# Optimization experiments

Hardware: AMD Instinct MI355X
Metric: run time of the kernel (lower is better)

The kernel has to match this reference:

```python
import jax, jax.numpy as jnp
import numpy as np

K_EXPERTS = 2  # init kwarg k_experts

def _glu_mlp(x, up_w, gate_w, down_w):
    # gated MLP: down( up(x) * GELU(gate(x)) ), exact-erf GELU matching torch nn.GELU()
    h = (x @ up_w) * jax.nn.gelu(x @ gate_w, approximate=False)
    return h @ down_w

def setup_inputs() -> dict:
    key = jax.random.key(0)
    ks = jax.random.split(key, 8)
    B, S, D, I, E = 2, 2048, 1024, 512, 8
    sc = 0.02
    return {
        "x": jax.random.normal(ks[0], (B, S, D), jnp.float32),
        "gate_w": jax.random.normal(ks[1], (E, D), jnp.float32) * sc,
        "up_w": jax.random.normal(ks[2], (E, D, I), jnp.float32) * sc,
        "gproj_w": jax.random.normal(ks[3], (E, D, I), jnp.float32) * sc,
        "down_w": jax.random.normal(ks[4], (E, I, D), jnp.float32) * sc,
        "shared_up_w": jax.random.normal(ks[5], (D, I), jnp.float32) * sc,
        "shared_gate_w": jax.random.normal(ks[6], (D, I), jnp.float32) * sc,
        "shared_down_w": jax.random.normal(ks[7], (I, D), jnp.float32) * sc,
    }

def reference(x, gate_w, up_w, gproj_w, down_w, shared_up_w, shared_gate_w, shared_down_w):
    B, S, D = x.shape
    E = gate_w.shape[0]
    xf = x.reshape(-1, D)                      # [T, D]
    T = xf.shape[0]

    # --- SigmaGate: softmax over expert logits, top-k, renormalize ---
    logits = xf @ gate_w.T                     # [T, E]
    scores = jax.nn.softmax(logits, axis=-1)
    topk_w, topk_idx = jax.lax.top_k(scores, K_EXPERTS)   # [T, k]
    topk_w = topk_w / (topk_w.sum(axis=-1, keepdims=True) + 1e-20)

    # combine weights as dense [T, E] (topk indices are distinct per token)
    combine = jnp.zeros((T, E), xf.dtype).at[jnp.arange(T)[:, None], topk_idx].add(topk_w)

    # --- experts: scan over E, accumulate weighted expert outputs ---
    def step(acc, ws):
        uw, gw, dw, ce = ws                    # ce: [T] combine weight for this expert
        y_e = _glu_mlp(xf, uw, gw, dw)         # [T, D]
        return acc + ce[:, None] * y_e, None

    y, _ = jax.lax.scan(step, jnp.zeros_like(xf), (up_w, gproj_w, down_w, combine.T))

    # --- shared expert on identity ---
    y = y + _glu_mlp(xf, shared_up_w, shared_gate_w, shared_down_w)
    return y.reshape(B, S, D)
```

## Files before the change

kernel.cpp:

```cpp
#include <hip/hip_runtime.h>
#include <hip/hip_bf16.h>
#include <math.h>

#define T_TOK 4096
#define D_DIM 1024
#define I_DIM 512
#define E_EXP 8
#define KSEL 2
#define NPAIR (T_TOK * KSEL)
#define ROUTED_CAP 9216
#define SHARED_BASE ROUTED_CAP
#define RTOT (ROUTED_CAP + T_TOK)
#define MAXTILES 104
#define GRID_G (MAXTILES * 8)

typedef __bf16 bf16x8 __attribute__((ext_vector_type(8)));
typedef float f32x4 __attribute__((ext_vector_type(4)));
typedef unsigned short ushort8 __attribute__((ext_vector_type(8)));

constexpr size_t SZ_XB  = (size_t)T_TOK * D_DIM * 2;
constexpr size_t SZ_UG  = (size_t)E_EXP * 2 * I_DIM * D_DIM * 2;
constexpr size_t SZ_DT  = (size_t)E_EXP * I_DIM * D_DIM * 2;
constexpr size_t SZ_SUG = (size_t)2 * I_DIM * D_DIM * 2;
constexpr size_t SZ_SDT = (size_t)I_DIM * D_DIM * 2;
constexpr size_t SZ_H   = (size_t)RTOT * I_DIM * 2;
constexpr size_t SZ_Y   = (size_t)RTOT * D_DIM * 2;

constexpr size_t OFF_XB   = 0;
constexpr size_t OFF_UG   = OFF_XB  + SZ_XB;
constexpr size_t OFF_DT   = OFF_UG  + SZ_UG;
constexpr size_t OFF_SUG  = OFF_DT  + SZ_DT;
constexpr size_t OFF_SDT  = OFF_SUG + SZ_SUG;
constexpr size_t OFF_H    = OFF_SDT + SZ_SDT;
constexpr size_t OFF_Y    = OFF_H   + SZ_H;
constexpr size_t OFF_TOPKI= OFF_Y   + SZ_Y;
constexpr size_t OFF_TOPKW= OFF_TOPKI + (size_t)NPAIR * 4;
constexpr size_t OFF_INV  = OFF_TOPKW + (size_t)NPAIR * 4;
constexpr size_t OFF_PERM = OFF_INV   + (size_t)NPAIR * 4;
constexpr size_t OFF_META = OFF_PERM  + (size_t)RTOT * 4;

__device__ __forceinline__ unsigned short f2bf(float f) {
  unsigned int u = __float_as_uint(f);
  unsigned int r = (u + 0x7FFFu + ((u >> 16) & 1u)) >> 16;
  return (unsigned short)r;
}
__device__ __forceinline__ float bf2f(unsigned short s) {
  return __uint_as_float(((unsigned int)s) << 16);
}
__device__ __forceinline__ void gload_lds16(const void* g, void* l) {
  __builtin_amdgcn_global_load_lds(
      (const __attribute__((address_space(1))) void*)g,
      (__attribute__((address_space(3))) void*)l, 16, 0, 0);
}

__global__ void transpose_cvt_all(
    const float* __restrict__ upw, const float* __restrict__ gpw,
    const float* __restrict__ dww, const float* __restrict__ sup,
    const float* __restrict__ sgt, const float* __restrict__ sdw,
    unsigned short* __restrict__ UG, unsigned short* __restrict__ sUG,
    unsigned short* __restrict__ Dt, unsigned short* __restrict__ sDt) {
  __shared__ float t[32][33];
  int bid = blockIdx.x;
  const float* in; unsigned short* out;
  int R, C, xt, yt, mode;
  if (bid < 4096)       { int e = bid >> 9, s = bid & 511;
    in = upw + (size_t)e * D_DIM * I_DIM; out = UG + (size_t)e * 2 * I_DIM * D_DIM;
    R = D_DIM; C = I_DIM; xt = s & 15; yt = s >> 4; mode = 0; }
  else if (bid < 8192)  { int b = bid - 4096; int e = b >> 9, s = b & 511;
    in = gpw + (size_t)e * D_DIM * I_DIM; out = UG + (size_t)e * 2 * I_DIM * D_DIM;
    R = D_DIM; C = I_DIM; xt = s & 15; yt = s >> 4; mode = 1; }
  else if (bid < 12288) { int b = bid - 8192; int e = b >> 9, s = b & 511;
    in = dww + (size_t)e * I_DIM * D_DIM; out = Dt + (size_t)e * I_DIM * D_DIM;
    R = I_DIM; C = D_DIM; xt = s & 31; yt = s >> 5; mode = 2; }
  else if (bid < 12800) { int s = bid - 12288;
    in = sup; out = sUG; R = D_DIM; C = I_DIM; xt = s & 15; yt = s >> 4; mode = 0; }
  else if (bid < 13312) { int s = bid - 12800;
    in = sgt; out = sUG; R = D_DIM; C = I_DIM; xt = s & 15; yt = s >> 4; mode = 1; }
  else                  { int s = bid - 13312;
    in = sdw; out = sDt; R = I_DIM; C = D_DIM; xt = s & 31; yt = s >> 5; mode = 2; }
  int c0 = xt * 32, r0 = yt * 32;
  int tx = threadIdx.x, ty = threadIdx.y;
#pragma unroll
  for (int i = 0; i < 4; ++i)
    t[ty + 8 * i][tx] = in[(size_t)(r0 + ty + 8 * i) * C + c0 + tx];
  __syncthreads();
#pragma unroll
  for (int i = 0; i < 4; ++i) {
    int c = c0 + ty + 8 * i;
    int orow = (mode == 2) ? c : (((c >> 4) << 5) + (c & 15) + (mode == 1 ? 16 : 0));
    out[(size_t)orow * R + r0 + tx] = f2bf(t[tx][ty + 8 * i]);
  }
}

__global__ void gating_kernel(const float* __restrict__ x, const float* __restrict__ gw,
                              unsigned short* __restrict__ xb,
                              int* __restrict__ topk_idx, float* __restrict__ topk_w) {
  int lane = threadIdx.x & 63;
  int t = blockIdx.x * 4 + (threadIdx.x >> 6);
  const float4* xr = (const float4*)(x + (size_t)t * D_DIM);
  float4 xv[4];
#pragma unroll
  for (int j = 0; j < 4; ++j) xv[j] = xr[lane + 64 * j];
#pragma unroll
  for (int j = 0; j < 4; ++j) {
    ushort4 o;
    o.x = f2bf(xv[j].x); o.y = f2bf(xv[j].y); o.z = f2bf(xv[j].z); o.w = f2bf(xv[j].w);
    *(ushort4*)&xb[(size_t)t * D_DIM + (lane + 64 * j) * 4] = o;
  }
  float acc[E_EXP];
#pragma unroll
  for (int e = 0; e < E_EXP; ++e) {
    const float4* gr = (const float4*)(gw + (size_t)e * D_DIM);
    float a = 0.f;
#pragma unroll
    for (int j = 0; j < 4; ++j) {
      float4 g = gr[lane + 64 * j];
      a += xv[j].x * g.x + xv[j].y * g.y + xv[j].z * g.z + xv[j].w * g.w;
    }
    acc[e] = a;
  }
#pragma unroll
  for (int off = 32; off; off >>= 1)
#pragma unroll
    for (int e = 0; e < E_EXP; ++e) acc[e] += __shfl_xor(acc[e], off, 64);
  if (lane == 0) {
    int i0 = 0; float m0 = acc[0];
#pragma unroll
    for (int e = 1; e < E_EXP; ++e) if (acc[e] > m0) { m0 = acc[e]; i0 = e; }
    int i1 = -1; float m1 = -1e30f;
#pragma unroll
    for (int e = 0; e < E_EXP; ++e) if (e != i0 && acc[e] > m1) { m1 = acc[e]; i1 = e; }
    float e1 = __expf(m1 - m0);
    float w0 = 1.0f / (1.0f + e1);
    float w1 = e1 / (1.0f + e1);
    topk_idx[2 * t] = i0; topk_idx[2 * t + 1] = i1;
    topk_w[2 * t] = w0;   topk_w[2 * t + 1] = w1;
  }
}

__global__ __launch_bounds__(1024) void route_kernel(
    const int* __restrict__ tidx, int* __restrict__ meta,
    int* __restrict__ perm, int* __restrict__ inv) {
  __shared__ int els[NPAIR];
  __shared__ int cnt_iw[128][E_EXP];
  __shared__ int base_iw[128][E_EXP];
  __shared__ int ebase[E_EXP];
  __shared__ int ecnt[E_EXP];
  int tid = threadIdx.x, lane = tid & 63, wv = tid >> 6;

  for (int it = 0; it < NPAIR / 1024; ++it) {
    int g = it * 1024 + tid;
    int e = tidx[g];
    els[g] = e;
#pragma unroll
    for (int ex = 0; ex < E_EXP; ++ex) {
      unsigned long long m = __ballot(e == ex);
      if (lane == 0) cnt_iw[it * 16 + wv][ex] = __popcll(m);
    }
  }
  __syncthreads();

  if (tid < E_EXP) {
    int s = 0;
    for (int iw = 0; iw < 128; ++iw) { base_iw[iw][tid] = s; s += cnt_iw[iw][tid]; }
    ecnt[tid] = s;
  }
  __syncthreads();

  if (tid == 0) {
    int o = 0, tc = 0;
    int2* m2 = (int2*)meta;
    for (int e = 0; e < E_EXP; ++e) {
      ebase[e] = o;
      int c = ecnt[e];
      int pt = (c + 127) >> 7;
      for (int ti = 0; ti < pt; ++ti) m2[tc++] = make_int2(e, o + ti * 128);
      o += pt * 128;
    }
    for (int ti = 0; ti < T_TOK / 128; ++ti)
      m2[tc++] = make_int2(E_EXP, SHARED_BASE + ti * 128);
    for (; tc < MAXTILES; ++tc) m2[tc] = make_int2(-1, 0);
  }
  __syncthreads();

  for (int it = 0; it < NPAIR / 1024; ++it) {
    int g = it * 1024 + tid;
    int e = els[g];
    int rank = 0;
#pragma unroll
    for (int ex = 0; ex < E_EXP; ++ex) {
      unsigned long long m = __ballot(e == ex);
      if (e == ex) rank = __popcll(m & ((1ull << lane) - 1ull));
    }
    int row = ebase[e] + base_iw[it * 16 + wv][e] + rank;
    perm[row] = g >> 1;
    inv[g] = row;
  }
  {
    int p = tid;
    int e = p >> 7, s = p & 127;
    int c = ecnt[e];
    int padn = (((c + 127) >> 7) << 7) - c;
    if (s < padn) perm[ebase[e] + c + s] = 0;
  }
  for (int t = tid; t < T_TOK; t += 1024) perm[SHARED_BASE + t] = t;
}

__global__ __launch_bounds__(256, 3) void gemm1_kernel(
    const unsigned short* __restrict__ xb, const unsigned short* __restrict__ UG,
    const unsigned short* __restrict__ sUG, unsigned short* __restrict__ H,
    const int* __restrict__ meta, const int* __restrict__ perm) {
  int orig = blockIdx.x;
  int wg = (orig & 7) * (GRID_G / 8) + (orig >> 3);
  int mt = wg >> 3, nt = wg & 7;
  int2 m2 = ((const int2*)meta)[mt];
  int e = m2.x;
  if (e < 0) return;
  int base = m2.y;
  int n0 = nt * 128;
  const unsigned short* B = (e < E_EXP) ? UG + (size_t)e * 2 * I_DIM * D_DIM : sUG;

  __shared__ unsigned short As[128 * 32];
  __shared__ unsigned short Bs[128 * 32];

  int tid = threadIdx.x, lane = tid & 63, wv = tid >> 6;
  int am0 = tid >> 2, ak0 = (tid & 3) * 8;
  int am1 = am0 + 64;
  int tok0 = perm[base + am0];
  int tok1 = perm[base + am1];
  const unsigned short* ga0 = xb + (size_t)tok0 * D_DIM + ak0;
  const unsigned short* ga1 = xb + (size_t)tok1 * D_DIM + ak0;
  const unsigned short* gb0 = B + (size_t)(n0 + am0) * D_DIM + ak0;
  const unsigned short* gb1 = B + (size_t)(n0 + am1) * D_DIM + ak0;
  unsigned short* lA0 = As + wv * 512; unsigned short* lA1 = As + 2048 + wv * 512;
  unsigned short* lB0 = Bs + wv * 512; unsigned short* lB1 = Bs + 2048 + wv * 512;

  f32x4 acc[4][4] = {};
  int wr = (wv >> 1) * 64, wc = (wv & 1) * 64;
  int l15 = lane & 15, l4 = lane >> 4;

  for (int k0 = 0; k0 < D_DIM; k0 += 32) {
    gload_lds16(ga0 + k0, lA0); gload_lds16(ga1 + k0, lA1);
    gload_lds16(gb0 + k0, lB0); gload_lds16(gb1 + k0, lB1);
    __syncthreads();
    bf16x8 af[4], bf[4];
#pragma unroll
    for (int i = 0; i < 4; ++i) {
      af[i] = *reinterpret_cast<const bf16x8*>(&As[(wr + i * 16 + l15) * 32 + l4 * 8]);
      bf[i] = *reinterpret_cast<const bf16x8*>(&Bs[(wc + i * 16 + l15) * 32 + l4 * 8]);
    }
#pragma unroll
    for (int i = 0; i < 4; ++i)
#pragma unroll
      for (int j = 0; j < 4; ++j)
        acc[i][j] = __builtin_amdgcn_mfma_f32_16x16x32_bf16(af[i], bf[j], acc[i][j], 0, 0, 0);
    __syncthreads();
  }

  const float is2 = 0.70710678118654752f;
  int hbase = (n0 >> 1) + (wv & 1) * 32;
#pragma unroll
  for (int i = 0; i < 4; ++i) {
    int row = base + wr + i * 16 + l4 * 4;
#pragma unroll
    for (int m = 0; m < 2; ++m) {
      int col = hbase + m * 16 + l15;
#pragma unroll
      for (int r = 0; r < 4; ++r) {
        float u = acc[i][2 * m][r], g = acc[i][2 * m + 1][r];
        float gl = 0.5f * g * (1.0f + erff(g * is2));
        H[(size_t)(row + r) * I_DIM + col] = f2bf(u * gl);
      }
    }
  }
}

__global__ __launch_bounds__(256, 3) void gemm2_kernel(
    const unsigned short* __restrict__ H, const unsigned short* __restrict__ Dt,
    const unsigned short* __restrict__ sDt, unsigned short* __restrict__ Y,
    const int* __restrict__ meta) {
  int orig = blockIdx.x;
  int wg = (orig & 7) * (GRID_G / 8) + (orig >> 3);
  int mt = wg >> 3, nt = wg & 7;
  int2 m2 = ((const int2*)meta)[mt];
  int e = m2.x;
  if (e < 0) return;
  int base = m2.y;
  int n0 = nt * 128;
  const unsigned short* B = (e < E_EXP) ? Dt + (size_t)e * D_DIM * I_DIM : sDt;

  __shared__ unsigned short As[128 * 32];
  __shared__ unsigned short Bs[128 * 32];

  int tid = threadIdx.x, lane = tid & 63, wv = tid >> 6;
  int am0 = tid >> 2, ak0 = (tid & 3) * 8;
  int am1 = am0 + 64;
  const unsigned short* ga0 = H + (size_t)(base + am0) * I_DIM + ak0;
  const unsigned short* ga1 = H + (size_t)(base + am1) * I_DIM + ak0;
  const unsigned short* gb0 = B + (size_t)(n0 + am0) * I_DIM + ak0;
  const unsigned short* gb1 = B + (size_t)(n0 + am1) * I_DIM + ak0;
  unsigned short* lA0 = As + wv * 512; unsigned short* lA1 = As + 2048 + wv * 512;
  unsigned short* lB0 = Bs + wv * 512; unsigned short* lB1 = Bs + 2048 + wv * 512;

  f32x4 acc[4][4] = {};
  int wr = (wv >> 1) * 64, wc = (wv & 1) * 64;
  int l15 = lane & 15, l4 = lane >> 4;

  for (int k0 = 0; k0 < I_DIM; k0 += 32) {
    gload_lds16(ga0 + k0, lA0); gload_lds16(ga1 + k0, lA1);
    gload_lds16(gb0 + k0, lB0); gload_lds16(gb1 + k0, lB1);
    __syncthreads();
    bf16x8 af[4], bf[4];
#pragma unroll
    for (int i = 0; i < 4; ++i) {
      af[i] = *reinterpret_cast<const bf16x8*>(&As[(wr + i * 16 + l15) * 32 + l4 * 8]);
      bf[i] = *reinterpret_cast<const bf16x8*>(&Bs[(wc + i * 16 + l15) * 32 + l4 * 8]);
    }
#pragma unroll
    for (int i = 0; i < 4; ++i)
#pragma unroll
      for (int j = 0; j < 4; ++j)
        acc[i][j] = __builtin_amdgcn_mfma_f32_16x16x32_bf16(af[i], bf[j], acc[i][j], 0, 0, 0);
    __syncthreads();
  }

#pragma unroll
  for (int i = 0; i < 4; ++i) {
    int row = base + wr + i * 16 + l4 * 4;
#pragma unroll
    for (int j = 0; j < 4; ++j) {
      int col = n0 + wc + j * 16 + l15;
#pragma unroll
      for (int r = 0; r < 4; ++r)
        Y[(size_t)(row + r) * D_DIM + col] = f2bf(acc[i][j][r]);
    }
  }
}

__global__ void combine_kernel(const unsigned short* __restrict__ Y, const int* __restrict__ inv,
                               const float* __restrict__ tw, float* __restrict__ out) {
  int g = blockIdx.x * 256 + threadIdx.x;
  int t = g >> 7, d0 = (g & 127) * 8;
  int r0 = inv[2 * t], r1 = inv[2 * t + 1];
  float w0 = tw[2 * t], w1 = tw[2 * t + 1];
  ushort8 y0 = *(const ushort8*)&Y[(size_t)r0 * D_DIM + d0];
  ushort8 y1 = *(const ushort8*)&Y[(size_t)r1 * D_DIM + d0];
  ushort8 ys = *(const ushort8*)&Y[(size_t)(SHARED_BASE + t) * D_DIM + d0];
  float o[8];
#pragma unroll
  for (int j = 0; j < 8; ++j)
    o[j] = w0 * bf2f(y0[j]) + w1 * bf2f(y1[j]) + bf2f(ys[j]);
  float4* op = (float4*)(out + (size_t)t * D_DIM + d0);
  op[0] = make_float4(o[0], o[1], o[2], o[3]);
  op[1] = make_float4(o[4], o[5], o[6], o[7]);
}

extern "C" void kernel_launch(void* const* d_in, const int* in_sizes, int n_in,
                              void* d_out, int out_size, void* d_ws, size_t ws_size,
                              hipStream_t stream) {
  const float* x    = (const float*)d_in[0];
  const float* gw   = (const float*)d_in[1];
  const float* upw  = (const float*)d_in[2];
  const float* gpw  = (const float*)d_in[3];
  const float* dww  = (const float*)d_in[4];
  const float* sup  = (const float*)d_in[5];
  const float* sgt  = (const float*)d_in[6];
  const float* sdw  = (const float*)d_in[7];
  float* out = (float*)d_out;

  char* ws = (char*)d_ws;
  unsigned short* xb  = (unsigned short*)(ws + OFF_XB);
  unsigned short* UG  = (unsigned short*)(ws + OFF_UG);
  unsigned short* Dt  = (unsigned short*)(ws + OFF_DT);
  unsigned short* sUG = (unsigned short*)(ws + OFF_SUG);
  unsigned short* sDt = (unsigned short*)(ws + OFF_SDT);
  unsigned short* H   = (unsigned short*)(ws + OFF_H);
  unsigned short* Y   = (unsigned short*)(ws + OFF_Y);
  int*   tki   = (int*)(ws + OFF_TOPKI);
  float* tkw   = (float*)(ws + OFF_TOPKW);
  int*   inv   = (int*)(ws + OFF_INV);
  int*   perm  = (int*)(ws + OFF_PERM);
  int*   meta  = (int*)(ws + OFF_META);

  transpose_cvt_all<<<13824, dim3(32, 8), 0, stream>>>(upw, gpw, dww, sup, sgt, sdw,
                                                       UG, sUG, Dt, sDt);
  gating_kernel<<<T_TOK / 4, 256, 0, stream>>>(x, gw, xb, tki, tkw);
  route_kernel<<<1, 1024, 0, stream>>>(tki, meta, perm, inv);

  gemm1_kernel<<<GRID_G, 256, 0, stream>>>(xb, UG, sUG, H, meta, perm);
  gemm2_kernel<<<GRID_G, 256, 0, stream>>>(H, Dt, sDt, Y, meta);
  combine_kernel<<<(T_TOK * 128) / 256, 256, 0, stream>>>(Y, inv, tkw, out);
}
```

Before: 116.9 us.

## Double K tile to 64 with XOR-swizzled LDS layout in both GEMMs

```diff
diff --git a/kernel.cpp b/kernel.cpp
--- a/kernel.cpp
+++ b/kernel.cpp
@@ -220,40 +220,47 @@
   int n0 = nt * 128;
   const unsigned short* B = (e < E_EXP) ? UG + (size_t)e * 2 * I_DIM * D_DIM : sUG;
 
-  __shared__ unsigned short As[128 * 32];
-  __shared__ unsigned short Bs[128 * 32];
+  __shared__ unsigned short As[128 * 64];
+  __shared__ unsigned short Bs[128 * 64];
 
   int tid = threadIdx.x, lane = tid & 63, wv = tid >> 6;
-  int am0 = tid >> 2, ak0 = (tid & 3) * 8;
-  int am1 = am0 + 64;
-  int tok0 = perm[base + am0];
-  int tok1 = perm[base + am1];
-  const unsigned short* ga0 = xb + (size_t)tok0 * D_DIM + ak0;
-  const unsigned short* ga1 = xb + (size_t)tok1 * D_DIM + ak0;
-  const unsigned short* gb0 = B + (size_t)(n0 + am0) * D_DIM + ak0;
-  const unsigned short* gb1 = B + (size_t)(n0 + am1) * D_DIM + ak0;
-  unsigned short* lA0 = As + wv * 512; unsigned short* lA1 = As + 2048 + wv * 512;
-  unsigned short* lB0 = Bs + wv * 512; unsigned short* lB1 = Bs + 2048 + wv * 512;
+  const unsigned short *gA[4], *gB[4];
+  unsigned short *lA[4], *lB[4];
+#pragma unroll
+  for (int j = 0; j < 4; ++j) {
+    int c = j * 256 + tid;
+    int row = c >> 3, q = c & 7, qs = q ^ (row & 7);
+    int tok = perm[base + row];
+    gA[j] = xb + (size_t)tok * D_DIM + qs * 8;
+    gB[j] = B + (size_t)(n0 + row) * D_DIM + qs * 8;
+    int dbase = (j * 256 + wv * 64) * 8;
+    lA[j] = As + dbase; lB[j] = Bs + dbase;
+  }
 
   f32x4 acc[4][4] = {};
   int wr = (wv >> 1) * 64, wc = (wv & 1) * 64;
   int l15 = lane & 15, l4 = lane >> 4;
-
-  for (int k0 = 0; k0 < D_DIM; k0 += 32) {
-    gload_lds16(ga0 + k0, lA0); gload_lds16(ga1 + k0, lA1);
-    gload_lds16(gb0 + k0, lB0); gload_lds16(gb1 + k0, lB1);
+  int sx = l15 & 7;
+
+  for (int k0 = 0; k0 < D_DIM; k0 += 64) {
+#pragma unroll
+    for (int j = 0; j < 4; ++j) { gload_lds16(gA[j] + k0, lA[j]); gload_lds16(gB[j] + k0, lB[j]); }
     __syncthreads();
-    bf16x8 af[4], bf[4];
-#pragma unroll
-    for (int i = 0; i < 4; ++i) {
-      af[i] = *reinterpret_cast<const bf16x8*>(&As[(wr + i * 16 + l15) * 32 + l4 * 8]);
-      bf[i] = *reinterpret_cast<const bf16x8*>(&Bs[(wc + i * 16 + l15) * 32 + l4 * 8]);
-    }
-#pragma unroll
-    for (int i = 0; i < 4; ++i)
-#pragma unroll
-      for (int j = 0; j < 4; ++j)
-        acc[i][j] = __builtin_amdgcn_mfma_f32_16x16x32_bf16(af[i], bf[j], acc[i][j], 0, 0, 0);
+#pragma unroll
+    for (int kh = 0; kh < 2; ++kh) {
+      bf16x8 af[4], bf[4];
+      int kb = kh * 4 + l4;
+#pragma unroll
+      for (int i = 0; i < 4; ++i) {
+        af[i] = *reinterpret_cast<const bf16x8*>(&As[(wr + i * 16 + l15) * 64 + (kb ^ sx) * 8]);
+        bf[i] = *reinterpret_cast<const bf16x8*>(&Bs[(wc + i * 16 + l15) * 64 + (kb ^ sx) * 8]);
+      }
+#pragma unroll
+      for (int i = 0; i < 4; ++i)
+#pragma unroll
+        for (int j = 0; j < 4; ++j)
+          acc[i][j] = __builtin_amdgcn_mfma_f32_16x16x32_bf16(af[i], bf[j], acc[i][j], 0, 0, 0);
+    }
     __syncthreads();
   }
 
@@ -289,38 +296,46 @@
   int n0 = nt * 128;
   const unsigned short* B = (e < E_EXP) ? Dt + (size_t)e * D_DIM * I_DIM : sDt;
 
-  __shared__ unsigned short As[128 * 32];
-  __shared__ unsigned short Bs[128 * 32];
+  __shared__ unsigned short As[128 * 64];
+  __shared__ unsigned short Bs[128 * 64];
 
   int tid = threadIdx.x, lane = tid & 63, wv = tid >> 6;
-  int am0 = tid >> 2, ak0 = (tid & 3) * 8;
-  int am1 = am0 + 64;
-  const unsigned short* ga0 = H + (size_t)(base + am0) * I_DIM + ak0;
-  const unsigned short* ga1 = H + (size_t)(base + am1) * I_DIM + ak0;
-  const unsigned short* gb0 = B + (size_t)(n0 + am0) * I_DIM + ak0;
-  const unsigned short* gb1 = B + (size_t)(n0 + am1) * I_DIM + ak0;
-  unsigned short* lA0 = As + wv * 512; unsigned short* lA1 = As + 2048 + wv * 512;
-  unsigned short* lB0 = Bs + wv * 512; unsigned short* lB1 = Bs + 2048 + wv * 512;
+  const unsigned short *gA[4], *gB[4];
+  unsigned short *lA[4], *lB[4];
+#pragma unroll
+  for (int j = 0; j < 4; ++j) {
+    int c = j * 256 + tid;
+    int row = c >> 3, q = c & 7, qs = q ^ (row & 7);
+    gA[j] = H + (size_t)(base + row) * I_DIM + qs * 8;
+    gB[j] = B + (size_t)(n0 + row) * I_DIM + qs * 8;
+    int dbase = (j * 256 + wv * 64) * 8;
+    lA[j] = As + dbase; lB[j] = Bs + dbase;
+  }
 
   f32x4 acc[4][4] = {};
   int wr = (wv >> 1) * 64, wc = (wv & 1) * 64;
   int l15 = lane & 15, l4 = lane >> 4;
-
-  for (int k0 = 0; k0 < I_DIM; k0 += 32) {
-    gload_lds16(ga0 + k0, lA0); gload_lds16(ga1 + k0, lA1);
-    gload_lds16(gb0 + k0, lB0); gload_lds16(gb1 + k0, lB1);
+  int sx = l15 & 7;
+
+  for (int k0 = 0; k0 < I_DIM; k0 += 64) {
+#pragma unroll
+    for (int j = 0; j < 4; ++j) { gload_lds16(gA[j] + k0, lA[j]); gload_lds16(gB[j] + k0, lB[j]); }
     __syncthreads();
-    bf16x8 af[4], bf[4];
-#pragma unroll
-    for (int i = 0; i < 4; ++i) {
-      af[i] = *reinterpret_cast<const bf16x8*>(&As[(wr + i * 16 + l15) * 32 + l4 * 8]);
-      bf[i] = *reinterpret_cast<const bf16x8*>(&Bs[(wc + i * 16 + l15) * 32 + l4 * 8]);
-    }
-#pragma unroll
-    for (int i = 0; i < 4; ++i)
-#pragma unroll
-      for (int j = 0; j < 4; ++j)
-        acc[i][j] = __builtin_amdgcn_mfma_f32_16x16x32_bf16(af[i], bf[j], acc[i][j], 0, 0, 0);
+#pragma unroll
+    for (int kh = 0; kh < 2; ++kh) {
+      bf16x8 af[4], bf[4];
+      int kb = kh * 4 + l4;
+#pragma unroll
+      for (int i = 0; i < 4; ++i) {
+        af[i] = *reinterpret_cast<const bf16x8*>(&As[(wr + i * 16 + l15) * 64 + (kb ^ sx) * 8]);
+        bf[i] = *reinterpret_cast<const bf16x8*>(&Bs[(wc + i * 16 + l15) * 64 + (kb ^ sx) * 8]);
+      }
+#pragma unroll
+      for (int i = 0; i < 4; ++i)
+#pragma unroll
+        for (int j = 0; j < 4; ++j)
+          acc[i][j] = __builtin_amdgcn_mfma_f32_16x16x32_bf16(af[i], bf[j], acc[i][j], 0, 0, 0);
+    }
     __syncthreads();
   }
 
```

Result: faster. 113.0 us (-3.3%).
